# Optimization experiments

Hardware: AMD Instinct MI355X
Metric: run time of the kernel (lower is better)

## Reference

```python
import jax, jax.numpy as jnp
import numpy as np
import math

# Static configuration (matches init_kwargs / input_specs)
L1 = 2          # lmax of x
L2 = 2          # lmax of y
LZ = L1 + L2    # output lmax = 4
RB = 20         # res_beta (Gauss-Legendre nodes)
RA = 19         # res_alpha (uniform azimuthal samples)
MUL = 128       # input multiplicity per l
C = 128         # num_channels
N = 1024        # batch (nodes/edges)


def _assoc_legendre(l, m, x):
    """Associated Legendre P_l^m(x) with Condon-Shortley phase, via recurrence."""
    pmm = np.ones_like(x)
    if m > 0:
        dfact = float(np.prod(np.arange(1, 2 * m, 2)))  # (2m-1)!!
        pmm = ((-1.0) ** m) * dfact * (1.0 - x * x) ** (m / 2.0)
    if l == m:
        return pmm
    pmmp1 = x * (2 * m + 1) * pmm
    if l == m + 1:
        return pmmp1
    for ll in range(m + 2, l + 1):
        p = ((2 * ll - 1) * x * pmmp1 - (ll + m - 1) * pmm) / (ll - m)
        pmm, pmmp1 = pmmp1, p
    return pmmp1


def _sh_table(L, rb, ra):
    """Orthonormal real spherical harmonics sampled on the (beta, alpha) grid.

    Returns Y [(L+1)^2, rb, ra] and Gauss-Legendre weights qw [rb] such that
    sum_{b,a} f(b,a) Y_lm(b,a) qw[b] * (2*pi/ra) == c_lm exactly for
    bandlimited f (the inverse of the synthesis c -> grid).
    """
    ct, qw = np.polynomial.legendre.leggauss(rb)  # nodes = cos(beta)
    alpha = 2.0 * np.pi * np.arange(ra) / ra
    Y = np.zeros(((L + 1) ** 2, rb, ra))
    for l in range(L + 1):
        for m in range(-l, l + 1):
            am = abs(m)
            nlm = math.sqrt((2 * l + 1) / (4 * math.pi)
                            * math.factorial(l - am) / math.factorial(l + am))
            P = _assoc_legendre(l, am, ct)  # [rb]
            if m == 0:
                ang = np.ones(ra)
            elif m > 0:
                ang = math.sqrt(2.0) * np.cos(m * alpha)
            else:
                ang = math.sqrt(2.0) * np.sin(am * alpha)
            Y[l * l + l + m] = nlm * P[:, None] * ang[None, :]
    return Y, qw


_Y_np, _QW_np = _sh_table(LZ, RB, RA)
Y_TAB = jnp.asarray(_Y_np, jnp.float32)   # [(LZ+1)^2, RB, RA]
QW = jnp.asarray(_QW_np, jnp.float32)     # [RB]


def _per_l_linear_in(v, w, L):
    """Equivariant per-l linear: v [N, mul, (L+1)^2], w [L+1, mul, C] -> [N, C, (L+1)^2]."""
    scale = 1.0 / math.sqrt(v.shape[1])
    outs = [jnp.einsum('nmd,mc->ncd', v[..., l * l:(l + 1) ** 2], w[l]) * scale
            for l in range(L + 1)]
    return jnp.concatenate(outs, axis=-1)


def setup_inputs() -> dict:
    key = jax.random.key(0)
    k0, k1, k2, k3, k4 = jax.random.split(key, 5)
    return {
        'x': jax.random.normal(k0, (N, MUL, (L1 + 1) ** 2), jnp.float32),
        'y': jax.random.normal(k1, (N, MUL, (L2 + 1) ** 2), jnp.float32),
        'wx': jax.random.normal(k2, (L1 + 1, MUL, C), jnp.float32),
        'wy': jax.random.normal(k3, (L2 + 1, MUL, C), jnp.float32),
        'wz': jax.random.normal(k4, (LZ + 1, C, C), jnp.float32),
    }


def reference(x, y, wx, wy, wz):
    # linear_in + mul_to_axis: [N, mul, D] -> [N, C, D]
    xc = _per_l_linear_in(x, wx, L1)  # [N, C, 9]
    yc = _per_l_linear_in(y, wy, L2)  # [N, C, 9]

    # to_s2grid (synthesis): coeffs -> signal on (beta, alpha) grid
    gx = jnp.einsum('ncd,dba->ncba', xc, Y_TAB[:(L1 + 1) ** 2])  # [N,C,RB,RA]
    gy = jnp.einsum('ncd,dba->ncba', yc, Y_TAB[:(L2 + 1) ** 2])

    # pointwise Gaunt product on the grid
    prod = gx * gy

    # from_s2grid (analysis): quadrature projection onto Y_lm up to LZ
    z = jnp.einsum('ncba,dba,b->ncd', prod, Y_TAB, QW) * (2.0 * jnp.pi / RA)  # [N,C,25]

    # axis_to_mul + linear_out_z: per-l channel mixing [C -> C]
    scale = 1.0 / math.sqrt(C)
    outs = [jnp.einsum('ncd,ce->ned', z[..., l * l:(l + 1) ** 2], wz[l]) * scale
            for l in range(LZ + 1)]
    return jnp.concatenate(outs, axis=-1)  # [N, C, 25]
```

## Files before the change

kernel.cpp:

```cpp
#include <hip/hip_runtime.h>
#include <cmath>

#define RB 20
#define RA 19
#define NPT (RB*RA)
#define DZ 25
#define DIN 9
#define MULT 128
#define CH 128

static void host_build_gaunt(float* out ) {
    const double PI = 3.14159265358979323846;
    double xq[RB], wq[RB];
    for (int i = 0; i < RB; ++i) {
        double x = cos(PI * (i + 0.75) / (RB + 0.5));
        double dp = 0.0;
        for (int it = 0; it < 100; ++it) {
            double p0 = 1.0, p1 = x;
            for (int k = 2; k <= RB; ++k) {
                double p2 = ((2.0*k - 1.0)*x*p1 - (k - 1.0)*p0) / (double)k;
                p0 = p1; p1 = p2;
            }
            dp = RB * (x*p1 - p0) / (x*x - 1.0);
            double dx = p1 / dp;
            x -= dx;
            if (fabs(dx) < 1e-15) break;
        }
        {
            double p0 = 1.0, p1 = x;
            for (int k = 2; k <= RB; ++k) {
                double p2 = ((2.0*k - 1.0)*x*p1 - (k - 1.0)*p0) / (double)k;
                p0 = p1; p1 = p2;
            }
            dp = RB * (x*p1 - p0) / (x*x - 1.0);
        }
        xq[i] = x;
        wq[i] = 2.0 / ((1.0 - x*x)*dp*dp);
    }
    static double Y[DZ][NPT];
    static double qws[NPT];
    for (int b = 0; b < RB; ++b) {
        double ct = xq[b], st = sqrt(fmax(0.0, 1.0 - ct*ct));
        double P[5][5]; double pmm = 1.0;
        for (int m = 0; m <= 4; ++m) {
            if (m > 0) pmm *= -(2.0*m - 1.0) * st;
            P[m][m] = pmm;
            if (m < 4) {
                double pp = pmm, pc = ct*(2.0*m + 1.0)*pmm;
                P[m+1][m] = pc;
                for (int l = m + 2; l <= 4; ++l) {
                    double pn = ((2.0*l - 1.0)*ct*pc - (double)(l + m - 1)*pp) / (double)(l - m);
                    P[l][m] = pn; pp = pc; pc = pn;
                }
            }
        }
        for (int a = 0; a < RA; ++a) {
            int pt = b*RA + a;
            qws[pt] = wq[b] * (2.0*PI/(double)RA);
            double alpha = 2.0*PI*(double)a/(double)RA;
            for (int l = 0; l <= 4; ++l)
                for (int m = -l; m <= l; ++m) {
                    int am = m < 0 ? -m : m;
                    double fr = 1.0;
                    for (int i = l - am + 1; i <= l + am; ++i) fr *= (double)i;
                    double nlm = sqrt((2.0*l + 1.0) / (4.0*PI) / fr);
                    double ang = (m == 0) ? 1.0
                               : (m > 0 ? sqrt(2.0)*cos(am*alpha) : sqrt(2.0)*sin(am*alpha));
                    Y[l*l + l + m][pt] = nlm * P[l][am] * ang;
                }
        }
    }
    for (int pr = 0; pr < 81; ++pr) {
        int d1 = pr / 9, d2 = pr % 9;
        for (int d = 0; d < DZ; ++d) {
            double s = 0.0;
            for (int p = 0; p < NPT; ++p)
                s += Y[d][p] * Y[d1][p] * Y[d2][p] * qws[p];
            out[pr*28 + d] = (float)s;
        }
    }
}

template<int D0, int ND>
__device__ __forceinline__ void d_tile(const float* sZ, const float* __restrict__ wz,
                                       float* sOut, int lane) {
    const float s128 = 0.08838834764831845f;
    float acc[ND * 4];
    #pragma unroll
    for (int i = 0; i < ND * 4; ++i) acc[i] = 0.f;
    for (int c0 = 0; c0 < CH; c0 += 4) {
        #pragma unroll
        for (int i = 0; i < ND; ++i) {
            const int d = D0 + i;
            const int l = (d == 0) ? 0 : (d < 4) ? 1 : (d < 9) ? 2 : (d < 16) ? 3 : 4;
            float4 z0 = *(const float4*)(sZ + d * 128 + c0);
            float4 z1 = *(const float4*)(sZ + (25 + d) * 128 + c0);
            #pragma unroll
            for (int k = 0; k < 4; ++k) {
                float wa = wz[l * 16384 + (c0 + k) * 128 + lane];
                float wb = wz[l * 16384 + (c0 + k) * 128 + lane + 64];
                float zc0 = (k == 0) ? z0.x : (k == 1) ? z0.y : (k == 2) ? z0.z : z0.w;
                float zc1 = (k == 0) ? z1.x : (k == 1) ? z1.y : (k == 2) ? z1.z : z1.w;
                acc[i*4+0] = fmaf(zc0, wa, acc[i*4+0]);
                acc[i*4+1] = fmaf(zc0, wb, acc[i*4+1]);
                acc[i*4+2] = fmaf(zc1, wa, acc[i*4+2]);
                acc[i*4+3] = fmaf(zc1, wb, acc[i*4+3]);
            }
        }
    }
    #pragma unroll
    for (int i = 0; i < ND; ++i) {
        sOut[(lane) * 25 + D0 + i]            = acc[i*4+0] * s128;
        sOut[(lane + 64) * 25 + D0 + i]       = acc[i*4+1] * s128;
        sOut[(128 + lane) * 25 + D0 + i]      = acc[i*4+2] * s128;
        sOut[(128 + lane + 64) * 25 + D0 + i] = acc[i*4+3] * s128;
    }
}

__global__ __launch_bounds__(256) void gaunt_fused(
    const float* __restrict__ xg, const float* __restrict__ yg,
    const float* __restrict__ wxg, const float* __restrict__ wyg,
    const float* __restrict__ wzg, float* __restrict__ outg,
    const float* __restrict__ gGt) {

    __shared__ __align__(16) float pool[15616];
    float* sZ   = pool;
    float* sXY  = pool + 6400;
    float* sG   = pool + 6400;
    float* sOut = pool + 6400;
    float* sXc  = pool + 11008;

    const int tid  = threadIdx.x;
    const int b    = blockIdx.x;
    const int lane = tid & 63;
    const int wave = __builtin_amdgcn_readfirstlane(tid >> 6);
    const float s128 = 0.08838834764831845f;

    {
        const float4* xs = (const float4*)(xg + 2 * b * 1152);
        const float4* ys = (const float4*)(yg + 2 * b * 1152);
        for (int i = tid; i < 1152; i += 256) {
            float4 v = (i < 576) ? xs[i] : ys[i - 576];
            int r = (i < 576) ? i : i - 576;
            int base = (i < 576) ? 0 : 2304;
            int j0 = r * 4;
            #pragma unroll
            for (int k = 0; k < 4; ++k) {
                int j = j0 + k;
                int n = j / 1152;
                int jj = j - n * 1152;
                int m = jj / 9, d = jj - 9 * m;
                float val = (k == 0) ? v.x : (k == 1) ? v.y : (k == 2) ? v.z : v.w;
                sXY[base + n * 1152 + d * 128 + m] = val;
            }
        }
    }
    __syncthreads();

    {
        const int side = wave >> 1, ch = wave & 1;
        const int c = ch * 64 + lane;
        const float* wb = side ? wyg : wxg;
        const float* xb = sXY + side * 2304;
        float acc[18];
        #pragma unroll
        for (int i = 0; i < 18; ++i) acc[i] = 0.f;
        for (int m0 = 0; m0 < MULT; m0 += 4) {
            float w0[4], w1[4], w2[4];
            #pragma unroll
            for (int k = 0; k < 4; ++k) {
                w0[k] = wb[(m0 + k) * 128 + c];
                w1[k] = wb[16384 + (m0 + k) * 128 + c];
                w2[k] = wb[32768 + (m0 + k) * 128 + c];
            }
            #pragma unroll
            for (int d = 0; d < 9; ++d) {
                const float* wl = (d == 0) ? w0 : (d < 4) ? w1 : w2;
                float4 x0 = *(const float4*)(xb + d * 128 + m0);
                float4 x1 = *(const float4*)(xb + 1152 + d * 128 + m0);
                acc[d*2+0] = fmaf(x0.x, wl[0], acc[d*2+0]);
                acc[d*2+0] = fmaf(x0.y, wl[1], acc[d*2+0]);
                acc[d*2+0] = fmaf(x0.z, wl[2], acc[d*2+0]);
                acc[d*2+0] = fmaf(x0.w, wl[3], acc[d*2+0]);
                acc[d*2+1] = fmaf(x1.x, wl[0], acc[d*2+1]);
                acc[d*2+1] = fmaf(x1.y, wl[1], acc[d*2+1]);
                acc[d*2+1] = fmaf(x1.z, wl[2], acc[d*2+1]);
                acc[d*2+1] = fmaf(x1.w, wl[3], acc[d*2+1]);
            }
        }
        #pragma unroll
        for (int d = 0; d < 9; ++d) {
            sXc[((side * 9 + d) * 2 + 0) * 128 + c] = acc[d*2+0] * s128;
            sXc[((side * 9 + d) * 2 + 1) * 128 + c] = acc[d*2+1] * s128;
        }
    }
    __syncthreads();

    for (int i = tid; i < 81 * 28; i += 256) sG[i] = gGt[i];
    __syncthreads();

    {
        const int c = tid & 127;
        const int half = __builtin_amdgcn_readfirstlane(tid >> 7);
        const int dz0 = half ? 12 : 0;
        float xr0[9], xr1[9], yr0[9], yr1[9];
        #pragma unroll
        for (int d = 0; d < 9; ++d) {
            xr0[d] = sXc[(d * 2 + 0) * 128 + c];
            xr1[d] = sXc[(d * 2 + 1) * 128 + c];
            yr0[d] = sXc[((9 + d) * 2 + 0) * 128 + c];
            yr1[d] = sXc[((9 + d) * 2 + 1) * 128 + c];
        }
        float a0[13], a1[13];
        #pragma unroll
        for (int i = 0; i < 13; ++i) { a0[i] = 0.f; a1[i] = 0.f; }
        for (int d1 = 0; d1 < 9; ++d1) {
            #pragma unroll
            for (int d2 = 0; d2 < 9; ++d2) {
                float p0 = xr0[d1] * yr0[d2];
                float p1 = xr1[d1] * yr1[d2];
                const float* gt = sG + (d1 * 9 + d2) * 28 + dz0;
                float4 g0 = *(const float4*)gt;
                float4 g1 = *(const float4*)(gt + 4);
                float4 g2 = *(const float4*)(gt + 8);
                float  g3 = gt[12];
                float gv[13] = {g0.x,g0.y,g0.z,g0.w, g1.x,g1.y,g1.z,g1.w,
                                g2.x,g2.y,g2.z,g2.w, g3};
                #pragma unroll
                for (int i = 0; i < 13; ++i) {
                    a0[i] = fmaf(p0, gv[i], a0[i]);
                    a1[i] = fmaf(p1, gv[i], a1[i]);
                }
            }
        }
        if (half == 0) {
            #pragma unroll
            for (int i = 0; i < 12; ++i) {
                sZ[i * 128 + c]        = a0[i];
                sZ[(25 + i) * 128 + c] = a1[i];
            }
        } else {
            #pragma unroll
            for (int i = 0; i < 13; ++i) {
                sZ[(12 + i) * 128 + c] = a0[i];
                sZ[(37 + i) * 128 + c] = a1[i];
            }
        }
    }
    __syncthreads();

    if      (wave == 0) d_tile<0, 4>(sZ, wzg, sOut, lane);
    else if (wave == 1) d_tile<4, 5>(sZ, wzg, sOut, lane);
    else if (wave == 2) d_tile<9, 7>(sZ, wzg, sOut, lane);
    else                d_tile<16, 9>(sZ, wzg, sOut, lane);
    __syncthreads();

    float* po = outg + 2 * b * (CH * DZ);
    const float4* so = (const float4*)sOut;
    for (int j = tid; j < (2 * CH * DZ) / 4; j += 256)
        ((float4*)po)[j] = so[j];
}

extern "C" void kernel_launch(void* const* d_in, const int* in_sizes, int n_in,
                              void* d_out, int out_size, void* d_ws, size_t ws_size,
                              hipStream_t stream) {
    static float h_gGt[81 * 28];
    host_build_gaunt(h_gGt);
    hipMemcpyAsync(d_ws, h_gGt, sizeof(h_gGt), hipMemcpyHostToDevice, stream);

    int N = in_sizes[0] / (MULT * DIN);

    hipLaunchKernelGGL(gaunt_fused, dim3(N / 2), dim3(256), 0, stream,
                       (const float*)d_in[0], (const float*)d_in[1],
                       (const float*)d_in[2], (const float*)d_in[3],
                       (const float*)d_in[4], (float*)d_out, (const float*)d_ws);
}
```

Before: 111.7 us.

## Double block size to 512 threads, one node per thread group

Changes the block from 256 to 512 threads so that each thread handles a single node instead of two in the input linear, Gaunt contraction and output linear stages. The shared-memory pool is re-laid out so the Gaunt table is loaded at kernel start alongside the inputs, which removes one barrier. This halves per-thread register accumulators and raises the number of threads per block. The cost is that weight loads from global memory are now duplicated across the two node groups instead of being reused in registers for both nodes. Shared memory per block also grows.

```diff
diff --git a/kernel.cpp b/kernel.cpp
--- a/kernel.cpp
+++ b/kernel.cpp
@@ -82,64 +82,59 @@
 }
 
 template<int D0, int ND>
-__device__ __forceinline__ void d_tile(const float* sZ, const float* __restrict__ wz,
-                                       float* sOut, int lane) {
+__device__ __forceinline__ void d_tile(const float* sZn, const float* __restrict__ wz,
+                                       float* sOutn, int lane) {
     const float s128 = 0.08838834764831845f;
-    float acc[ND * 4];
+    float acc[ND * 2];
     #pragma unroll
-    for (int i = 0; i < ND * 4; ++i) acc[i] = 0.f;
+    for (int i = 0; i < ND * 2; ++i) acc[i] = 0.f;
     for (int c0 = 0; c0 < CH; c0 += 4) {
         #pragma unroll
         for (int i = 0; i < ND; ++i) {
             const int d = D0 + i;
             const int l = (d == 0) ? 0 : (d < 4) ? 1 : (d < 9) ? 2 : (d < 16) ? 3 : 4;
-            float4 z0 = *(const float4*)(sZ + d * 128 + c0);
-            float4 z1 = *(const float4*)(sZ + (25 + d) * 128 + c0);
+            float4 z = *(const float4*)(sZn + d * 128 + c0);
             #pragma unroll
             for (int k = 0; k < 4; ++k) {
                 float wa = wz[l * 16384 + (c0 + k) * 128 + lane];
                 float wb = wz[l * 16384 + (c0 + k) * 128 + lane + 64];
-                float zc0 = (k == 0) ? z0.x : (k == 1) ? z0.y : (k == 2) ? z0.z : z0.w;
-                float zc1 = (k == 0) ? z1.x : (k == 1) ? z1.y : (k == 2) ? z1.z : z1.w;
-                acc[i*4+0] = fmaf(zc0, wa, acc[i*4+0]);
-                acc[i*4+1] = fmaf(zc0, wb, acc[i*4+1]);
-                acc[i*4+2] = fmaf(zc1, wa, acc[i*4+2]);
-                acc[i*4+3] = fmaf(zc1, wb, acc[i*4+3]);
+                float zc = (k == 0) ? z.x : (k == 1) ? z.y : (k == 2) ? z.z : z.w;
+                acc[i*2+0] = fmaf(zc, wa, acc[i*2+0]);
+                acc[i*2+1] = fmaf(zc, wb, acc[i*2+1]);
             }
         }
     }
     #pragma unroll
     for (int i = 0; i < ND; ++i) {
-        sOut[(lane) * 25 + D0 + i]            = acc[i*4+0] * s128;
-        sOut[(lane + 64) * 25 + D0 + i]       = acc[i*4+1] * s128;
-        sOut[(128 + lane) * 25 + D0 + i]      = acc[i*4+2] * s128;
-        sOut[(128 + lane + 64) * 25 + D0 + i] = acc[i*4+3] * s128;
-    }
-}
-
-__global__ __launch_bounds__(256) void gaunt_fused(
+        sOutn[lane * 25 + D0 + i]        = acc[i*2+0] * s128;
+        sOutn[(lane + 64) * 25 + D0 + i] = acc[i*2+1] * s128;
+    }
+}
+
+__global__ __launch_bounds__(512) void gaunt_fused(
     const float* __restrict__ xg, const float* __restrict__ yg,
     const float* __restrict__ wxg, const float* __restrict__ wyg,
     const float* __restrict__ wzg, float* __restrict__ outg,
     const float* __restrict__ gGt) {
 
-    __shared__ __align__(16) float pool[15616];
-    float* sZ   = pool;
-    float* sXY  = pool + 6400;
-    float* sG   = pool + 6400;
-    float* sOut = pool + 6400;
-    float* sXc  = pool + 11008;
+    __shared__ __align__(16) float pool[17884];
+    float* sG   = pool;
+    float* sXY  = pool + 2268;
+    float* sXc  = pool + 6876;
+    float* sZ   = pool + 11484;
+    float* sOut = pool + 2268;
 
     const int tid  = threadIdx.x;
     const int b    = blockIdx.x;
     const int lane = tid & 63;
-    const int wave = __builtin_amdgcn_readfirstlane(tid >> 6);
+    const int wv   = __builtin_amdgcn_readfirstlane(tid >> 6);
     const float s128 = 0.08838834764831845f;
 
+    for (int i = tid; i < 81 * 28; i += 512) sG[i] = gGt[i];
     {
         const float4* xs = (const float4*)(xg + 2 * b * 1152);
         const float4* ys = (const float4*)(yg + 2 * b * 1152);
-        for (int i = tid; i < 1152; i += 256) {
+        for (int i = tid; i < 1152; i += 512) {
             float4 v = (i < 576) ? xs[i] : ys[i - 576];
             int r = (i < 576) ? i : i - 576;
             int base = (i < 576) ? 0 : 2304;
@@ -158,13 +153,15 @@
     __syncthreads();
 
     {
-        const int side = wave >> 1, ch = wave & 1;
-        const int c = ch * 64 + lane;
+        const int side = wv >> 2;
+        const int cq = wv & 3;
+        const int c = cq * 32 + (lane & 31);
+        const int n = lane >> 5;
         const float* wb = side ? wyg : wxg;
-        const float* xb = sXY + side * 2304;
-        float acc[18];
-        #pragma unroll
-        for (int i = 0; i < 18; ++i) acc[i] = 0.f;
+        const float* xb = sXY + side * 2304 + n * 1152;
+        float acc[9];
+        #pragma unroll
+        for (int d = 0; d < 9; ++d) acc[d] = 0.f;
         for (int m0 = 0; m0 < MULT; m0 += 4) {
             float w0[4], w1[4], w2[4];
             #pragma unroll
@@ -176,49 +173,37 @@
             #pragma unroll
             for (int d = 0; d < 9; ++d) {
                 const float* wl = (d == 0) ? w0 : (d < 4) ? w1 : w2;
-                float4 x0 = *(const float4*)(xb + d * 128 + m0);
-                float4 x1 = *(const float4*)(xb + 1152 + d * 128 + m0);
-                acc[d*2+0] = fmaf(x0.x, wl[0], acc[d*2+0]);
-                acc[d*2+0] = fmaf(x0.y, wl[1], acc[d*2+0]);
-                acc[d*2+0] = fmaf(x0.z, wl[2], acc[d*2+0]);
-                acc[d*2+0] = fmaf(x0.w, wl[3], acc[d*2+0]);
-                acc[d*2+1] = fmaf(x1.x, wl[0], acc[d*2+1]);
-                acc[d*2+1] = fmaf(x1.y, wl[1], acc[d*2+1]);
-                acc[d*2+1] = fmaf(x1.z, wl[2], acc[d*2+1]);
-                acc[d*2+1] = fmaf(x1.w, wl[3], acc[d*2+1]);
-            }
-        }
+                float4 xv = *(const float4*)(xb + d * 128 + m0);
+                acc[d] = fmaf(xv.x, wl[0], acc[d]);
+                acc[d] = fmaf(xv.y, wl[1], acc[d]);
+                acc[d] = fmaf(xv.z, wl[2], acc[d]);
+                acc[d] = fmaf(xv.w, wl[3], acc[d]);
+            }
+        }
+        #pragma unroll
+        for (int d = 0; d < 9; ++d)
+            sXc[((side * 9 + d) * 2 + n) * 128 + c] = acc[d] * s128;
+    }
+    __syncthreads();
+
+    {
+        const int c = tid & 127;
+        const int n = (tid >> 7) & 1;
+        const int half = __builtin_amdgcn_readfirstlane(tid >> 8);
+        const int dz0 = half ? 12 : 0;
+        float xr[9], yr[9];
         #pragma unroll
         for (int d = 0; d < 9; ++d) {
-            sXc[((side * 9 + d) * 2 + 0) * 128 + c] = acc[d*2+0] * s128;
-            sXc[((side * 9 + d) * 2 + 1) * 128 + c] = acc[d*2+1] * s128;
-        }
-    }
-    __syncthreads();
-
-    for (int i = tid; i < 81 * 28; i += 256) sG[i] = gGt[i];
-    __syncthreads();
-
-    {
-        const int c = tid & 127;
-        const int half = __builtin_amdgcn_readfirstlane(tid >> 7);
-        const int dz0 = half ? 12 : 0;
-        float xr0[9], xr1[9], yr0[9], yr1[9];
-        #pragma unroll
-        for (int d = 0; d < 9; ++d) {
-            xr0[d] = sXc[(d * 2 + 0) * 128 + c];
-            xr1[d] = sXc[(d * 2 + 1) * 128 + c];
-            yr0[d] = sXc[((9 + d) * 2 + 0) * 128 + c];
-            yr1[d] = sXc[((9 + d) * 2 + 1) * 128 + c];
-        }
-        float a0[13], a1[13];
-        #pragma unroll
-        for (int i = 0; i < 13; ++i) { a0[i] = 0.f; a1[i] = 0.f; }
+            xr[d] = sXc[(d * 2 + n) * 128 + c];
+            yr[d] = sXc[((9 + d) * 2 + n) * 128 + c];
+        }
+        float a[13];
+        #pragma unroll
+        for (int i = 0; i < 13; ++i) a[i] = 0.f;
         for (int d1 = 0; d1 < 9; ++d1) {
             #pragma unroll
             for (int d2 = 0; d2 < 9; ++d2) {
-                float p0 = xr0[d1] * yr0[d2];
-                float p1 = xr1[d1] * yr1[d2];
+                float p = xr[d1] * yr[d2];
                 const float* gt = sG + (d1 * 9 + d2) * 28 + dz0;
                 float4 g0 = *(const float4*)gt;
                 float4 g1 = *(const float4*)(gt + 4);
@@ -227,37 +212,35 @@
                 float gv[13] = {g0.x,g0.y,g0.z,g0.w, g1.x,g1.y,g1.z,g1.w,
                                 g2.x,g2.y,g2.z,g2.w, g3};
                 #pragma unroll
-                for (int i = 0; i < 13; ++i) {
-                    a0[i] = fmaf(p0, gv[i], a0[i]);
-                    a1[i] = fmaf(p1, gv[i], a1[i]);
-                }
-            }
-        }
+                for (int i = 0; i < 13; ++i) a[i] = fmaf(p, gv[i], a[i]);
+            }
+        }
+        float* zn = sZ + n * 25 * 128;
         if (half == 0) {
             #pragma unroll
-            for (int i = 0; i < 12; ++i) {
-                sZ[i * 128 + c]        = a0[i];
-                sZ[(25 + i) * 128 + c] = a1[i];
-            }
+            for (int i = 0; i < 12; ++i) zn[i * 128 + c] = a[i];
         } else {
             #pragma unroll
-            for (int i = 0; i < 13; ++i) {
-                sZ[(12 + i) * 128 + c] = a0[i];
-                sZ[(37 + i) * 128 + c] = a1[i];
-            }
-        }
-    }
-    __syncthreads();
-
-    if      (wave == 0) d_tile<0, 4>(sZ, wzg, sOut, lane);
-    else if (wave == 1) d_tile<4, 5>(sZ, wzg, sOut, lane);
-    else if (wave == 2) d_tile<9, 7>(sZ, wzg, sOut, lane);
-    else                d_tile<16, 9>(sZ, wzg, sOut, lane);
+            for (int i = 0; i < 13; ++i) zn[(12 + i) * 128 + c] = a[i];
+        }
+    }
+    __syncthreads();
+
+    {
+        const int n = wv >> 2;
+        const int dr = wv & 3;
+        const float* zn = sZ + n * 25 * 128;
+        float* on = sOut + n * 3200;
+        if      (dr == 0) d_tile<0, 4>(zn, wzg, on, lane);
+        else if (dr == 1) d_tile<4, 5>(zn, wzg, on, lane);
+        else if (dr == 2) d_tile<9, 7>(zn, wzg, on, lane);
+        else              d_tile<16, 9>(zn, wzg, on, lane);
+    }
     __syncthreads();
 
     float* po = outg + 2 * b * (CH * DZ);
     const float4* so = (const float4*)sOut;
-    for (int j = tid; j < (2 * CH * DZ) / 4; j += 256)
+    for (int j = tid; j < (2 * CH * DZ) / 4; j += 512)
         ((float4*)po)[j] = so[j];
 }
 
@@ -270,7 +253,7 @@
 
     int N = in_sizes[0] / (MULT * DIN);
 
-    hipLaunchKernelGGL(gaunt_fused, dim3(N / 2), dim3(256), 0, stream,
+    hipLaunchKernelGGL(gaunt_fused, dim3(N / 2), dim3(512), 0, stream,
                        (const float*)d_in[0], (const float*)d_in[1],
                        (const float*)d_in[2], (const float*)d_in[3],
                        (const float*)d_in[4], (float*)d_out, (const float*)d_ws);
```

Result: slower. 124.9 us (+11.8%).
